# Optimization experiments

Measured on AMD Instinct MI355X. Metric: run time of the kernel, lower is better.

## Reference

```python
import jax, jax.numpy as jnp
import numpy as np

N_TOKENS = 16384
HIDDEN = 1024
FFN = 256
N_EXPERTS = 12
TOP_K = 3


def setup_inputs() -> dict:
    key = jax.random.key(0)
    ks = jax.random.split(key, 5)
    return {
        "hidden_states": jax.random.normal(ks[0], (N_TOKENS, HIDDEN), dtype=jnp.float32),
        "gate_w": jax.random.normal(ks[1], (N_EXPERTS, HIDDEN), dtype=jnp.float32) * 0.02,
        "w1": jax.random.normal(ks[2], (N_EXPERTS, FFN, HIDDEN), dtype=jnp.float32) * 0.02,
        "w2": jax.random.normal(ks[3], (N_EXPERTS, HIDDEN, FFN), dtype=jnp.float32) * 0.02,
        "w3": jax.random.normal(ks[4], (N_EXPERTS, FFN, HIDDEN), dtype=jnp.float32) * 0.02,
    }


def reference(hidden_states, gate_w, w1, w2, w3):
    # Eval mode: no jitter noise (module only applies it when self.training).
    n = hidden_states.shape[0]
    router_logits = hidden_states @ gate_w.T                       # [N, E]
    routing_weights = jax.nn.softmax(router_logits.astype(jnp.float32), axis=1)
    top_w, selected_experts = jax.lax.top_k(routing_weights, TOP_K)  # [N, K]
    top_w = top_w / jnp.sum(top_w, axis=-1, keepdims=True)
    top_w = top_w.astype(hidden_states.dtype)

    # Dense combine-weight matrix [N, E]: zero for unselected experts.
    combine = jnp.zeros((n, N_EXPERTS), dtype=hidden_states.dtype)
    combine = combine.at[jnp.arange(n)[:, None], selected_experts].add(top_w)

    # SwiGLU experts computed for all (token, expert) pairs; unselected pairs
    # are zeroed by the combine weights -> same math as gather/scatter loop.
    h1 = jnp.einsum('nd,efd->nef', hidden_states, w1)              # [N, E, F]
    h3 = jnp.einsum('nd,efd->nef', hidden_states, w3)              # [N, E, F]
    h = jax.nn.silu(h1) * h3
    h = h * combine[:, :, None]                                    # weight before combine
    final = jnp.einsum('nef,edf->nd', h, w2)                       # [N, D]

    flat_e = selected_experts.reshape(-1)
    flat_w = top_w.reshape(-1).astype(jnp.float32)
    importance = jnp.zeros((N_EXPERTS,), jnp.float32).at[flat_e].add(flat_w)
    # torch.std is unbiased (ddof=1)
    router_loss = jnp.std(importance, ddof=1)
    return final, router_logits, selected_experts, router_loss
```

## Files before the change

kernel.cpp:

```cpp
#include <hip/hip_runtime.h>
#include <hip/hip_bf16.h>

#define NT 16384
#define HID 1024
#define FFN_ 256
#define NE 12
#define TOPK 3

typedef float  float4x  __attribute__((ext_vector_type(4)));
typedef short  short8x  __attribute__((ext_vector_type(8)));

__device__ __forceinline__ unsigned short f2bf(float f) {
    unsigned u = __float_as_uint(f);
    u += 0x7fffu + ((u >> 16) & 1u);
    return (unsigned short)(u >> 16);
}
__device__ __forceinline__ float bf2f(unsigned short u) {
    return __uint_as_float(((unsigned)u) << 16);
}

__device__ __forceinline__ void gl2lds16(const void* g, void* l) {
    __builtin_amdgcn_global_load_lds(
        (const __attribute__((address_space(1))) unsigned int*)g,
        (__attribute__((address_space(3))) unsigned int*)l, 16, 0, 0);
}

__global__ __launch_bounds__(256) void router_cvt_kernel(
    const float* __restrict__ X, const float* __restrict__ G,
    const float* __restrict__ w1, const float* __restrict__ w3, const float* __restrict__ w2,
    unsigned short* __restrict__ o1, unsigned short* __restrict__ o3, unsigned short* __restrict__ o2,
    float* __restrict__ out_logits, float* __restrict__ out_sel,
    unsigned short* __restrict__ xb,
    int* __restrict__ sel_e, float* __restrict__ sel_w)
{
    __shared__ __align__(16) float gls[NE * HID];

    if (blockIdx.x < 768) {
        const float* s; unsigned short* d;
        int m = blockIdx.x >> 8;
        if (m == 0)      { s = w1; d = o1; }
        else if (m == 1) { s = w3; d = o3; }
        else             { s = w2; d = o2; }
        const int n4 = NE * FFN_ * HID / 4;
        for (int i = (blockIdx.x & 255) * 256 + threadIdx.x; i < n4; i += 65536) {
            float4 v = ((const float4*)s)[i];
            ushort4 o;
            o.x = f2bf(v.x); o.y = f2bf(v.y); o.z = f2bf(v.z); o.w = f2bf(v.w);
            ((ushort4*)d)[i] = o;
        }
        return;
    }

    const int bx = blockIdx.x - 768;
    for (int i = threadIdx.x; i < NE * HID / 4; i += 256)
        ((float4*)gls)[i] = ((const float4*)G)[i];
    __syncthreads();

    const int wave = threadIdx.x >> 6, lane = threadIdx.x & 63;
    const int t = bx * 4 + wave;

    float xr[16];
    const float* xt = X + (size_t)t * HID;
    unsigned short* xbt = xb + (size_t)t * HID;
#pragma unroll
    for (int j = 0; j < 4; j++) {
        float4 v = ((const float4*)xt)[j * 64 + lane];
        xr[j*4+0] = v.x; xr[j*4+1] = v.y; xr[j*4+2] = v.z; xr[j*4+3] = v.w;
        ushort4 o;
        o.x = f2bf(v.x); o.y = f2bf(v.y); o.z = f2bf(v.z); o.w = f2bf(v.w);
        ((ushort4*)xbt)[j * 64 + lane] = o;
    }

    float logit[NE];
#pragma unroll
    for (int e = 0; e < NE; e++) {
        float s = 0.f;
#pragma unroll
        for (int j = 0; j < 4; j++) {
            float4 g = ((const float4*)gls)[e * 256 + j * 64 + lane];
            s += xr[j*4+0]*g.x + xr[j*4+1]*g.y + xr[j*4+2]*g.z + xr[j*4+3]*g.w;
        }
#pragma unroll
        for (int d = 32; d; d >>= 1) s += __shfl_xor(s, d, 64);
        logit[e] = s;
    }

    if (lane == 0) {
        float m = logit[0];
#pragma unroll
        for (int e = 1; e < NE; e++) m = fmaxf(m, logit[e]);
#pragma unroll
        for (int e = 0; e < NE; e++) out_logits[(size_t)t * NE + e] = logit[e];

        bool used[NE];
#pragma unroll
        for (int e = 0; e < NE; e++) used[e] = false;
        int   sel[TOPK];
        float w[TOPK];
        float wsum = 0.f;
#pragma unroll
        for (int k = 0; k < TOPK; k++) {
            int best = -1; float bv = -1e30f;
            for (int e = 0; e < NE; e++)
                if (!used[e] && logit[e] > bv) { bv = logit[e]; best = e; }
            used[best] = true;
            sel[k] = best;
            w[k] = __expf(bv - m);
            wsum += w[k];
        }
        float inv = 1.f / wsum;
#pragma unroll
        for (int k = 0; k < TOPK; k++) {
            float wk = w[k] * inv;
            out_sel[(size_t)t * TOPK + k] = (float)sel[k];
            sel_e[t * TOPK + k] = sel[k];
            sel_w[t * TOPK + k] = wk;
        }
    }
}

__global__ __launch_bounds__(256) void hist_kernel(
    const int* __restrict__ sel_e, const float* __restrict__ sel_w,
    int* __restrict__ counts, float* __restrict__ importance)
{
    __shared__ int   lcnt[NE];
    __shared__ float limp[NE];
    const int tid = threadIdx.x;
    if (tid < NE) { lcnt[tid] = 0; limp[tid] = 0.f; }
    __syncthreads();
    const int t = blockIdx.x * 256 + tid;
#pragma unroll
    for (int k = 0; k < TOPK; k++) {
        int e = sel_e[t * TOPK + k];
        atomicAdd(&lcnt[e], 1);
        atomicAdd(&limp[e], sel_w[t * TOPK + k]);
    }
    __syncthreads();
    if (tid < NE) {
        atomicAdd(&counts[tid], lcnt[tid]);
        atomicAdd(&importance[tid], limp[tid]);
    }
}

__global__ void scan_loss(const int* __restrict__ counts, int* __restrict__ cursor,
                          int* __restrict__ offsets, const float* __restrict__ importance,
                          float* __restrict__ loss_out)
{
    if (threadIdx.x == 0) {
        int acc = 0;
        for (int e = 0; e < NE; e++) { offsets[e] = acc; cursor[e] = acc; acc += counts[e]; }
        offsets[NE] = acc;
        float mean = 0.f;
        for (int e = 0; e < NE; e++) mean += importance[e];
        mean /= (float)NE;
        float var = 0.f;
        for (int e = 0; e < NE; e++) { float d = importance[e] - mean; var += d * d; }
        var /= (float)(NE - 1);
        *loss_out = sqrtf(var);
    }
}

__global__ __launch_bounds__(256) void place_kernel(
    const int* __restrict__ sel_e, const float* __restrict__ sel_w,
    int* __restrict__ cursor, int* __restrict__ tok_ids, float* __restrict__ slot_w,
    int* __restrict__ inv3)
{
    __shared__ int lcnt[NE];
    __shared__ int lbase[NE];
    const int tid = threadIdx.x;
    if (tid < NE) lcnt[tid] = 0;
    __syncthreads();
    const int t = blockIdx.x * 256 + tid;
    int e[TOPK], r[TOPK];
#pragma unroll
    for (int k = 0; k < TOPK; k++) {
        e[k] = sel_e[t * TOPK + k];
        r[k] = atomicAdd(&lcnt[e[k]], 1);
    }
    __syncthreads();
    if (tid < NE) lbase[tid] = atomicAdd(&cursor[tid], lcnt[tid]);
    __syncthreads();
#pragma unroll
    for (int k = 0; k < TOPK; k++) {
        int pos = lbase[e[k]] + r[k];
        tok_ids[pos] = t;
        slot_w[pos] = sel_w[t * TOPK + k];
        inv3[t * TOPK + k] = pos;
    }
}

__global__ __launch_bounds__(256) void ffn1_kernel(
    const unsigned short* __restrict__ xb, const unsigned short* __restrict__ wb1,
    const unsigned short* __restrict__ wb3, const int* __restrict__ offsets,
    const int* __restrict__ tok_ids, const float* __restrict__ slot_w,
    unsigned short* __restrict__ H)
{
    const int e = blockIdx.z;
    const int base = offsets[e];
    const int count = offsets[e + 1] - base;
    const int m0 = blockIdx.x * 128;
    if (m0 >= count) return;
    const int n0 = blockIdx.y * 128;

    __shared__ __align__(16) unsigned short As[128 * 32];
    __shared__ __align__(16) unsigned short B1s[128 * 32];
    __shared__ __align__(16) unsigned short B3s[128 * 32];
    __shared__ int   tids[128];
    __shared__ float wts[128];

    const int tid = threadIdx.x;
    if (tid < 128) {
        int s = m0 + tid;
        tids[tid] = (s < count) ? tok_ids[base + s] : 0;
        wts[tid]  = (s < count) ? slot_w[base + s] : 0.f;
    }
    __syncthreads();

    const int wave = tid >> 6, lane = tid & 63;
    const int wave_m = wave & 1, wave_n = wave >> 1;

    const int srow = wave * 32 + (lane >> 2);
    const int schunk = (((lane & 3) ^ ((srow >> 1) & 3)) << 3);
    const int tokA0 = tids[srow];
    const int tokA1 = tids[srow + 16];

    const unsigned short* asrc0 = xb + (size_t)tokA0 * HID + schunk;
    const unsigned short* asrc1 = xb + (size_t)tokA1 * HID + schunk;
    const unsigned short* b1p0 = wb1 + (size_t)(e * FFN_ + n0 + srow) * HID + schunk;
    const unsigned short* b1p1 = b1p0 + 16 * HID;
    const unsigned short* b3p0 = wb3 + (size_t)(e * FFN_ + n0 + srow) * HID + schunk;
    const unsigned short* b3p1 = b3p0 + 16 * HID;

    char* aD0  = (char*)As  + wave * 2048;  char* aD1  = aD0 + 1024;
    char* b1D0 = (char*)B1s + wave * 2048;  char* b1D1 = b1D0 + 1024;
    char* b3D0 = (char*)B3s + wave * 2048;  char* b3D1 = b3D0 + 1024;

    const int r15 = lane & 15;
    const int rchunk = (((lane >> 4) ^ ((r15 >> 1) & 3)) << 3);

    float4x acc1[4][4], acc3[4][4];
#pragma unroll
    for (int mi = 0; mi < 4; mi++)
#pragma unroll
        for (int ni = 0; ni < 4; ni++) {
            acc1[mi][ni] = (float4x){0.f, 0.f, 0.f, 0.f};
            acc3[mi][ni] = (float4x){0.f, 0.f, 0.f, 0.f};
        }

    for (int kk = 0; kk < HID / 32; kk++) {
        __syncthreads();
        gl2lds16(asrc0, aD0);  gl2lds16(asrc1, aD1);
        gl2lds16(b1p0, b1D0);  gl2lds16(b1p1, b1D1);
        gl2lds16(b3p0, b3D0);  gl2lds16(b3p1, b3D1);
        __syncthreads();
        asrc0 += 32; asrc1 += 32; b1p0 += 32; b1p1 += 32; b3p0 += 32; b3p1 += 32;

        short8x a[4], b1f[4], b3f[4];
#pragma unroll
        for (int mi = 0; mi < 4; mi++)
            a[mi] = *(const short8x*)(As + (wave_m * 64 + mi * 16 + r15) * 32 + rchunk);
#pragma unroll
        for (int ni = 0; ni < 4; ni++) {
            b1f[ni] = *(const short8x*)(B1s + (wave_n * 64 + ni * 16 + r15) * 32 + rchunk);
            b3f[ni] = *(const short8x*)(B3s + (wave_n * 64 + ni * 16 + r15) * 32 + rchunk);
        }
#pragma unroll
        for (int mi = 0; mi < 4; mi++)
#pragma unroll
            for (int ni = 0; ni < 4; ni++) {
                acc1[mi][ni] = __builtin_amdgcn_mfma_f32_16x16x32_bf16(a[mi], b1f[ni], acc1[mi][ni], 0, 0, 0);
                acc3[mi][ni] = __builtin_amdgcn_mfma_f32_16x16x32_bf16(a[mi], b3f[ni], acc3[mi][ni], 0, 0, 0);
            }
    }

    const int laneh = lane >> 4;
#pragma unroll
    for (int mi = 0; mi < 4; mi++)
#pragma unroll
        for (int ni = 0; ni < 4; ni++)
#pragma unroll
            for (int r = 0; r < 4; r++) {
                int ml = wave_m * 64 + mi * 16 + laneh * 4 + r;
                int s = m0 + ml;
                if (s < count) {
                    float v1 = acc1[mi][ni][r];
                    float v3 = acc3[mi][ni][r];
                    float h = v1 * (1.f / (1.f + __expf(-v1))) * v3 * wts[ml];
                    int n = n0 + wave_n * 64 + ni * 16 + r15;
                    H[(size_t)(base + s) * FFN_ + n] = f2bf(h);
                }
            }
}

__global__ __launch_bounds__(256) void ffn2_store(
    const unsigned short* __restrict__ H, const unsigned short* __restrict__ wb2,
    const int* __restrict__ offsets, unsigned short* __restrict__ Obuf,
    int co, int nc)
{
    const int e = blockIdx.z;
    const int base = offsets[e];
    const int count = offsets[e + 1] - base;
    const int m0 = blockIdx.x * 128;
    if (m0 >= count) return;
    const int n0g = co + blockIdx.y * 128;

    __shared__ __align__(16) unsigned short As[128 * 32];
    __shared__ __align__(16) unsigned short Bs[128 * 32];

    const int tid = threadIdx.x;
    const int wave = tid >> 6, lane = tid & 63;
    const int wave_m = wave & 1, wave_n = wave >> 1;

    const int srow = wave * 32 + (lane >> 2);
    const int schunk = (((lane & 3) ^ ((srow >> 1) & 3)) << 3);

    const unsigned short* a0 = H + (size_t)(base + m0 + srow) * FFN_ + schunk;
    const unsigned short* a1 = a0 + 16 * FFN_;
    const unsigned short* b0 = wb2 + (size_t)(e * HID + n0g + srow) * FFN_ + schunk;
    const unsigned short* b1 = b0 + 16 * FFN_;

    char* aD0 = (char*)As + wave * 2048;  char* aD1 = aD0 + 1024;
    char* bD0 = (char*)Bs + wave * 2048;  char* bD1 = bD0 + 1024;

    const int r15 = lane & 15;
    const int rchunk = (((lane >> 4) ^ ((r15 >> 1) & 3)) << 3);

    float4x acc[4][4];
#pragma unroll
    for (int mi = 0; mi < 4; mi++)
#pragma unroll
        for (int ni = 0; ni < 4; ni++) acc[mi][ni] = (float4x){0.f, 0.f, 0.f, 0.f};

    for (int kk = 0; kk < FFN_ / 32; kk++) {
        __syncthreads();
        gl2lds16(a0, aD0);  gl2lds16(a1, aD1);
        gl2lds16(b0, bD0);  gl2lds16(b1, bD1);
        __syncthreads();
        a0 += 32; a1 += 32; b0 += 32; b1 += 32;

        short8x af[4], bf[4];
#pragma unroll
        for (int mi = 0; mi < 4; mi++)
            af[mi] = *(const short8x*)(As + (wave_m * 64 + mi * 16 + r15) * 32 + rchunk);
#pragma unroll
        for (int ni = 0; ni < 4; ni++)
            bf[ni] = *(const short8x*)(Bs + (wave_n * 64 + ni * 16 + r15) * 32 + rchunk);
#pragma unroll
        for (int mi = 0; mi < 4; mi++)
#pragma unroll
            for (int ni = 0; ni < 4; ni++)
                acc[mi][ni] = __builtin_amdgcn_mfma_f32_16x16x32_bf16(af[mi], bf[ni], acc[mi][ni], 0, 0, 0);
    }

    const int laneh = lane >> 4;
#pragma unroll
    for (int mi = 0; mi < 4; mi++)
#pragma unroll
        for (int ni = 0; ni < 4; ni++)
#pragma unroll
            for (int r = 0; r < 4; r++) {
                int ml = wave_m * 64 + mi * 16 + laneh * 4 + r;
                int s = m0 + ml;
                if (s < count) {
                    int col = (n0g - co) + wave_n * 64 + ni * 16 + r15;
                    Obuf[(size_t)(base + s) * nc + col] = f2bf(acc[mi][ni][r]);
                }
            }
}

__global__ __launch_bounds__(256) void combine_kernel(
    const unsigned short* __restrict__ Obuf, const int* __restrict__ inv3,
    float* __restrict__ final_out, int co, int pt_shift)
{
    const int idx = blockIdx.x * 256 + threadIdx.x;
    const int per_t = 1 << pt_shift;
    const int t = idx >> pt_shift;
    const int c4 = idx & (per_t - 1);
    const int s0 = inv3[t * TOPK + 0];
    const int s1 = inv3[t * TOPK + 1];
    const int s2 = inv3[t * TOPK + 2];
    const ushort4* O = (const ushort4*)Obuf;
    ushort4 u0 = O[(size_t)s0 * per_t + c4];
    ushort4 u1 = O[(size_t)s1 * per_t + c4];
    ushort4 u2 = O[(size_t)s2 * per_t + c4];
    float4 r;
    r.x = bf2f(u0.x) + bf2f(u1.x) + bf2f(u2.x);
    r.y = bf2f(u0.y) + bf2f(u1.y) + bf2f(u2.y);
    r.z = bf2f(u0.z) + bf2f(u1.z) + bf2f(u2.z);
    r.w = bf2f(u0.w) + bf2f(u1.w) + bf2f(u2.w);
    ((float4*)(final_out + (size_t)t * HID + co))[c4] = r;
}

__global__ __launch_bounds__(256) void ffn2_atomic(
    const unsigned short* __restrict__ H, const unsigned short* __restrict__ wb2,
    const int* __restrict__ offsets, const int* __restrict__ tok_ids,
    float* __restrict__ final_out)
{
    const int e = blockIdx.z;
    const int base = offsets[e];
    const int count = offsets[e + 1] - base;
    const int m0 = blockIdx.x * 128;
    if (m0 >= count) return;
    const int n0 = blockIdx.y * 128;

    __shared__ __align__(16) unsigned short As[128 * 32];
    __shared__ __align__(16) unsigned short Bs[128 * 32];
    __shared__ int tids[128];

    const int tid = threadIdx.x;
    if (tid < 128) {
        int s = m0 + tid;
        tids[tid] = (s < count) ? tok_ids[base + s] : 0;
    }
    __syncthreads();

    const int wave = tid >> 6, lane = tid & 63;
    const int wave_m = wave & 1, wave_n = wave >> 1;

    const int srow = wave * 32 + (lane >> 2);
    const int schunk = (((lane & 3) ^ ((srow >> 1) & 3)) << 3);
    const unsigned short* a0 = H + (size_t)(base + m0 + srow) * FFN_ + schunk;
    const unsigned short* a1 = a0 + 16 * FFN_;
    const unsigned short* b0 = wb2 + (size_t)(e * HID + n0 + srow) * FFN_ + schunk;
    const unsigned short* b1 = b0 + 16 * FFN_;

    char* aD0 = (char*)As + wave * 2048;  char* aD1 = aD0 + 1024;
    char* bD0 = (char*)Bs + wave * 2048;  char* bD1 = bD0 + 1024;

    const int r15 = lane & 15;
    const int rchunk = (((lane >> 4) ^ ((r15 >> 1) & 3)) << 3);

    float4x acc[4][4];
#pragma unroll
    for (int mi = 0; mi < 4; mi++)
#pragma unroll
        for (int ni = 0; ni < 4; ni++) acc[mi][ni] = (float4x){0.f, 0.f, 0.f, 0.f};

    for (int kk = 0; kk < FFN_ / 32; kk++) {
        __syncthreads();
        gl2lds16(a0, aD0);  gl2lds16(a1, aD1);
        gl2lds16(b0, bD0);  gl2lds16(b1, bD1);
        __syncthreads();
        a0 += 32; a1 += 32; b0 += 32; b1 += 32;

        short8x af[4], bf[4];
#pragma unroll
        for (int mi = 0; mi < 4; mi++)
            af[mi] = *(const short8x*)(As + (wave_m * 64 + mi * 16 + r15) * 32 + rchunk);
#pragma unroll
        for (int ni = 0; ni < 4; ni++)
            bf[ni] = *(const short8x*)(Bs + (wave_n * 64 + ni * 16 + r15) * 32 + rchunk);
#pragma unroll
        for (int mi = 0; mi < 4; mi++)
#pragma unroll
            for (int ni = 0; ni < 4; ni++)
                acc[mi][ni] = __builtin_amdgcn_mfma_f32_16x16x32_bf16(af[mi], bf[ni], acc[mi][ni], 0, 0, 0);
    }

    const int laneh = lane >> 4;
#pragma unroll
    for (int mi = 0; mi < 4; mi++)
#pragma unroll
        for (int ni = 0; ni < 4; ni++)
#pragma unroll
            for (int r = 0; r < 4; r++) {
                int ml = wave_m * 64 + mi * 16 + laneh * 4 + r;
                int s = m0 + ml;
                if (s < count) {
                    int n = n0 + wave_n * 64 + ni * 16 + r15;
                    atomicAdd(final_out + (size_t)tids[ml] * HID + n, acc[mi][ni][r]);
                }
            }
}

extern "C" void kernel_launch(void* const* d_in, const int* in_sizes, int n_in,
                              void* d_out, int out_size, void* d_ws, size_t ws_size,
                              hipStream_t stream) {
    const float* X  = (const float*)d_in[0];
    const float* G  = (const float*)d_in[1];
    const float* w1 = (const float*)d_in[2];
    const float* w2 = (const float*)d_in[3];
    const float* w3 = (const float*)d_in[4];

    float* out = (float*)d_out;
    float* out_final  = out;
    float* out_logits = out + (size_t)NT * HID;
    float* out_sel    = out_logits + (size_t)NT * NE;
    float* out_loss   = out_sel + (size_t)NT * TOPK;

    char* ws = (char*)d_ws;
    int*   counts     = (int*)(ws + 0);
    int*   cursor     = (int*)(ws + 64);
    int*   offsets    = (int*)(ws + 128);
    float* importance = (float*)(ws + 192);
    int*   sel_e   = (int*)(ws + 512);
    float* sel_w   = (float*)(ws + 197120);
    int*   tok_ids = (int*)(ws + 393728);
    float* slot_w  = (float*)(ws + 590336);
    unsigned short* wb1 = (unsigned short*)(ws + 786944);
    unsigned short* wb3 = (unsigned short*)(ws + 7078400);
    unsigned short* wb2 = (unsigned short*)(ws + 13369856);
    unsigned short* H   = (unsigned short*)(ws + 19661312);
    int*  inv3          = (int*)(ws + 44892672);
    const size_t obase  = 45089280;
    unsigned short* Obuf = (unsigned short*)(ws + obase);

    unsigned short* xb = (unsigned short*)d_out;

    int nc = 0;
    if      (ws_size >= obase + (size_t)NT * TOPK * 1024 * 2) nc = 1024;
    else if (ws_size >= obase + (size_t)NT * TOPK * 512  * 2) nc = 512;
    else if (ws_size >= obase + (size_t)NT * TOPK * 256  * 2) nc = 256;

    hipMemsetAsync(ws, 0, 256, stream);
    router_cvt_kernel<<<768 + NT / 4, 256, 0, stream>>>(
        X, G, w1, w3, w2, wb1, wb3, wb2, out_logits, out_sel, xb, sel_e, sel_w);
    hist_kernel<<<NT / 256, 256, 0, stream>>>(sel_e, sel_w, counts, importance);
    scan_loss<<<1, 64, 0, stream>>>(counts, cursor, offsets, importance, out_loss);
    place_kernel<<<NT / 256, 256, 0, stream>>>(sel_e, sel_w, cursor, tok_ids, slot_w, inv3);
    ffn1_kernel<<<dim3(48, 2, NE), 256, 0, stream>>>(xb, wb1, wb3, offsets, tok_ids, slot_w, H);

    if (nc) {
        const int np = 1024 / nc;
        const int pt_shift = (nc == 1024) ? 8 : (nc == 512 ? 7 : 6);
        for (int p = 0; p < np; p++) {
            ffn2_store<<<dim3(48, nc / 128, NE), 256, 0, stream>>>(
                H, wb2, offsets, Obuf, p * nc, nc);
            combine_kernel<<<(NT << pt_shift) / 256, 256, 0, stream>>>(
                Obuf, inv3, out_final, p * nc, pt_shift);
        }
    } else {
        hipMemsetAsync(d_out, 0, (size_t)NT * HID * sizeof(float), stream);
        ffn2_atomic<<<dim3(48, 8, NE), 256, 0, stream>>>(H, wb2, offsets, tok_ids, out_final);
    }
}
```

Baseline: 390.5 us.

## Double-buffer LDS tiles in expert GEMMs and compact grid via per-expert tile prefix

Each of the three expert GEMM kernels now uses two LDS stages. The next K-slice is loaded while the current one is consumed, removing one barrier per iteration. The launch grid is flattened to a compact list of 128-row tiles, using a tile_base prefix computed in scan_loss, so the many empty per-expert blocks are no longer launched. This doubles LDS per block and adds a small expert lookup loop per block.

```diff
diff --git a/kernel.cpp b/kernel.cpp
--- a/kernel.cpp
+++ b/kernel.cpp
@@ -143,13 +143,19 @@
 }
 
 __global__ void scan_loss(const int* __restrict__ counts, int* __restrict__ cursor,
-                          int* __restrict__ offsets, const float* __restrict__ importance,
+                          int* __restrict__ offsets, int* __restrict__ tile_base,
+                          const float* __restrict__ importance,
                           float* __restrict__ loss_out)
 {
     if (threadIdx.x == 0) {
-        int acc = 0;
-        for (int e = 0; e < NE; e++) { offsets[e] = acc; cursor[e] = acc; acc += counts[e]; }
+        int acc = 0, tb = 0;
+        for (int e = 0; e < NE; e++) {
+            offsets[e] = acc; cursor[e] = acc; tile_base[e] = tb;
+            tb += (counts[e] + 127) >> 7;
+            acc += counts[e];
+        }
         offsets[NE] = acc;
+        tile_base[NE] = tb;
         float mean = 0.f;
         for (int e = 0; e < NE; e++) mean += importance[e];
         mean /= (float)NE;
@@ -192,19 +198,22 @@
 __global__ __launch_bounds__(256) void ffn1_kernel(
     const unsigned short* __restrict__ xb, const unsigned short* __restrict__ wb1,
     const unsigned short* __restrict__ wb3, const int* __restrict__ offsets,
+    const int* __restrict__ tile_base,
     const int* __restrict__ tok_ids, const float* __restrict__ slot_w,
     unsigned short* __restrict__ H)
 {
-    const int e = blockIdx.z;
+    const int bx = blockIdx.x;
+    if (bx >= tile_base[NE]) return;
+    int e = 0;
+    while (bx >= tile_base[e + 1]) e++;
     const int base = offsets[e];
     const int count = offsets[e + 1] - base;
-    const int m0 = blockIdx.x * 128;
-    if (m0 >= count) return;
+    const int m0 = (bx - tile_base[e]) << 7;
     const int n0 = blockIdx.y * 128;
 
-    __shared__ __align__(16) unsigned short As[128 * 32];
-    __shared__ __align__(16) unsigned short B1s[128 * 32];
-    __shared__ __align__(16) unsigned short B3s[128 * 32];
+    __shared__ __align__(16) unsigned short As[2][4096];
+    __shared__ __align__(16) unsigned short B1s[2][4096];
+    __shared__ __align__(16) unsigned short B3s[2][4096];
     __shared__ int   tids[128];
     __shared__ float wts[128];
 
@@ -231,9 +240,17 @@
     const unsigned short* b3p0 = wb3 + (size_t)(e * FFN_ + n0 + srow) * HID + schunk;
     const unsigned short* b3p1 = b3p0 + 16 * HID;
 
-    char* aD0  = (char*)As  + wave * 2048;  char* aD1  = aD0 + 1024;
-    char* b1D0 = (char*)B1s + wave * 2048;  char* b1D1 = b1D0 + 1024;
-    char* b3D0 = (char*)B3s + wave * 2048;  char* b3D1 = b3D0 + 1024;
+    const int woff = wave * 2048;
+
+#define FFN1_STAGE(p) do {                                             \
+        char* aD  = (char*)&As[p][0]  + woff;                          \
+        char* b1D = (char*)&B1s[p][0] + woff;                          \
+        char* b3D = (char*)&B3s[p][0] + woff;                          \
+        gl2lds16(asrc0, aD);  gl2lds16(asrc1, aD + 1024);              \
+        gl2lds16(b1p0, b1D);  gl2lds16(b1p1, b1D + 1024);              \
+        gl2lds16(b3p0, b3D);  gl2lds16(b3p1, b3D + 1024);              \
+        asrc0 += 32; asrc1 += 32; b1p0 += 32; b1p1 += 32;              \
+        b3p0 += 32; b3p1 += 32; } while (0)
 
     const int r15 = lane & 15;
     const int rchunk = (((lane >> 4) ^ ((r15 >> 1) & 3)) << 3);
@@ -247,22 +264,20 @@
             acc3[mi][ni] = (float4x){0.f, 0.f, 0.f, 0.f};
         }
 
+    FFN1_STAGE(0);
     for (int kk = 0; kk < HID / 32; kk++) {
         __syncthreads();
-        gl2lds16(asrc0, aD0);  gl2lds16(asrc1, aD1);
-        gl2lds16(b1p0, b1D0);  gl2lds16(b1p1, b1D1);
-        gl2lds16(b3p0, b3D0);  gl2lds16(b3p1, b3D1);
-        __syncthreads();
-        asrc0 += 32; asrc1 += 32; b1p0 += 32; b1p1 += 32; b3p0 += 32; b3p1 += 32;
+        if (kk + 1 < HID / 32) FFN1_STAGE((kk + 1) & 1);
+        const int p = kk & 1;
 
         short8x a[4], b1f[4], b3f[4];
 #pragma unroll
         for (int mi = 0; mi < 4; mi++)
-            a[mi] = *(const short8x*)(As + (wave_m * 64 + mi * 16 + r15) * 32 + rchunk);
+            a[mi] = *(const short8x*)(&As[p][0] + (wave_m * 64 + mi * 16 + r15) * 32 + rchunk);
 #pragma unroll
         for (int ni = 0; ni < 4; ni++) {
-            b1f[ni] = *(const short8x*)(B1s + (wave_n * 64 + ni * 16 + r15) * 32 + rchunk);
-            b3f[ni] = *(const short8x*)(B3s + (wave_n * 64 + ni * 16 + r15) * 32 + rchunk);
+            b1f[ni] = *(const short8x*)(&B1s[p][0] + (wave_n * 64 + ni * 16 + r15) * 32 + rchunk);
+            b3f[ni] = *(const short8x*)(&B3s[p][0] + (wave_n * 64 + ni * 16 + r15) * 32 + rchunk);
         }
 #pragma unroll
         for (int mi = 0; mi < 4; mi++)
@@ -272,6 +287,7 @@
                 acc3[mi][ni] = __builtin_amdgcn_mfma_f32_16x16x32_bf16(a[mi], b3f[ni], acc3[mi][ni], 0, 0, 0);
             }
     }
+#undef FFN1_STAGE
 
     const int laneh = lane >> 4;
 #pragma unroll
@@ -294,18 +310,20 @@
 
 __global__ __launch_bounds__(256) void ffn2_store(
     const unsigned short* __restrict__ H, const unsigned short* __restrict__ wb2,
-    const int* __restrict__ offsets, unsigned short* __restrict__ Obuf,
-    int co, int nc)
-{
-    const int e = blockIdx.z;
+    const int* __restrict__ offsets, const int* __restrict__ tile_base,
+    unsigned short* __restrict__ Obuf, int co, int nc)
+{
+    const int bx = blockIdx.x;
+    if (bx >= tile_base[NE]) return;
+    int e = 0;
+    while (bx >= tile_base[e + 1]) e++;
     const int base = offsets[e];
     const int count = offsets[e + 1] - base;
-    const int m0 = blockIdx.x * 128;
-    if (m0 >= count) return;
+    const int m0 = (bx - tile_base[e]) << 7;
     const int n0g = co + blockIdx.y * 128;
 
-    __shared__ __align__(16) unsigned short As[128 * 32];
-    __shared__ __align__(16) unsigned short Bs[128 * 32];
+    __shared__ __align__(16) unsigned short As[2][4096];
+    __shared__ __align__(16) unsigned short Bs[2][4096];
 
     const int tid = threadIdx.x;
     const int wave = tid >> 6, lane = tid & 63;
@@ -319,8 +337,14 @@
     const unsigned short* b0 = wb2 + (size_t)(e * HID + n0g + srow) * FFN_ + schunk;
     const unsigned short* b1 = b0 + 16 * FFN_;
 
-    char* aD0 = (char*)As + wave * 2048;  char* aD1 = aD0 + 1024;
-    char* bD0 = (char*)Bs + wave * 2048;  char* bD1 = bD0 + 1024;
+    const int woff = wave * 2048;
+
+#define FFN2_STAGE(p) do {                                             \
+        char* aD = (char*)&As[p][0] + woff;                            \
+        char* bD = (char*)&Bs[p][0] + woff;                            \
+        gl2lds16(a0, aD);  gl2lds16(a1, aD + 1024);                    \
+        gl2lds16(b0, bD);  gl2lds16(b1, bD + 1024);                    \
+        a0 += 32; a1 += 32; b0 += 32; b1 += 32; } while (0)
 
     const int r15 = lane & 15;
     const int rchunk = (((lane >> 4) ^ ((r15 >> 1) & 3)) << 3);
@@ -331,26 +355,26 @@
 #pragma unroll
         for (int ni = 0; ni < 4; ni++) acc[mi][ni] = (float4x){0.f, 0.f, 0.f, 0.f};
 
+    FFN2_STAGE(0);
     for (int kk = 0; kk < FFN_ / 32; kk++) {
         __syncthreads();
-        gl2lds16(a0, aD0);  gl2lds16(a1, aD1);
-        gl2lds16(b0, bD0);  gl2lds16(b1, bD1);
-        __syncthreads();
-        a0 += 32; a1 += 32; b0 += 32; b1 += 32;
+        if (kk + 1 < FFN_ / 32) FFN2_STAGE((kk + 1) & 1);
+        const int p = kk & 1;
 
         short8x af[4], bf[4];
 #pragma unroll
         for (int mi = 0; mi < 4; mi++)
-            af[mi] = *(const short8x*)(As + (wave_m * 64 + mi * 16 + r15) * 32 + rchunk);
+            af[mi] = *(const short8x*)(&As[p][0] + (wave_m * 64 + mi * 16 + r15) * 32 + rchunk);
 #pragma unroll
         for (int ni = 0; ni < 4; ni++)
-            bf[ni] = *(const short8x*)(Bs + (wave_n * 64 + ni * 16 + r15) * 32 + rchunk);
+            bf[ni] = *(const short8x*)(&Bs[p][0] + (wave_n * 64 + ni * 16 + r15) * 32 + rchunk);
 #pragma unroll
         for (int mi = 0; mi < 4; mi++)
 #pragma unroll
             for (int ni = 0; ni < 4; ni++)
                 acc[mi][ni] = __builtin_amdgcn_mfma_f32_16x16x32_bf16(af[mi], bf[ni], acc[mi][ni], 0, 0, 0);
     }
+#undef FFN2_STAGE
 
     const int laneh = lane >> 4;
 #pragma unroll
@@ -393,18 +417,20 @@
 
 __global__ __launch_bounds__(256) void ffn2_atomic(
     const unsigned short* __restrict__ H, const unsigned short* __restrict__ wb2,
-    const int* __restrict__ offsets, const int* __restrict__ tok_ids,
-    float* __restrict__ final_out)
-{
-    const int e = blockIdx.z;
+    const int* __restrict__ offsets, const int* __restrict__ tile_base,
+    const int* __restrict__ tok_ids, float* __restrict__ final_out)
+{
+    const int bx = blockIdx.x;
+    if (bx >= tile_base[NE]) return;
+    int e = 0;
+    while (bx >= tile_base[e + 1]) e++;
     const int base = offsets[e];
     const int count = offsets[e + 1] - base;
-    const int m0 = blockIdx.x * 128;
-    if (m0 >= count) return;
+    const int m0 = (bx - tile_base[e]) << 7;
     const int n0 = blockIdx.y * 128;
 
-    __shared__ __align__(16) unsigned short As[128 * 32];
-    __shared__ __align__(16) unsigned short Bs[128 * 32];
+    __shared__ __align__(16) unsigned short As[2][4096];
+    __shared__ __align__(16) unsigned short Bs[2][4096];
     __shared__ int tids[128];
 
     const int tid = threadIdx.x;
@@ -424,8 +450,13 @@
     const unsigned short* b0 = wb2 + (size_t)(e * HID + n0 + srow) * FFN_ + schunk;
     const unsigned short* b1 = b0 + 16 * FFN_;
 
-    char* aD0 = (char*)As + wave * 2048;  char* aD1 = aD0 + 1024;
-    char* bD0 = (char*)Bs + wave * 2048;  char* bD1 = bD0 + 1024;
+    const int woff = wave * 2048;
+#define FFN2A_STAGE(p) do {                                            \
+        char* aD = (char*)&As[p][0] + woff;                            \
+        char* bD = (char*)&Bs[p][0] + woff;                            \
+        gl2lds16(a0, aD);  gl2lds16(a1, aD + 1024);                    \
+        gl2lds16(b0, bD);  gl2lds16(b1, bD + 1024);                    \
+        a0 += 32; a1 += 32; b0 += 32; b1 += 32; } while (0)
 
     const int r15 = lane & 15;
     const int rchunk = (((lane >> 4) ^ ((r15 >> 1) & 3)) << 3);
@@ -436,26 +467,25 @@
 #pragma unroll
         for (int ni = 0; ni < 4; ni++) acc[mi][ni] = (float4x){0.f, 0.f, 0.f, 0.f};
 
+    FFN2A_STAGE(0);
     for (int kk = 0; kk < FFN_ / 32; kk++) {
         __syncthreads();
-        gl2lds16(a0, aD0);  gl2lds16(a1, aD1);
-        gl2lds16(b0, bD0);  gl2lds16(b1, bD1);
-        __syncthreads();
-        a0 += 32; a1 += 32; b0 += 32; b1 += 32;
-
+        if (kk + 1 < FFN_ / 32) FFN2A_STAGE((kk + 1) & 1);
+        const int p = kk & 1;
         short8x af[4], bf[4];
 #pragma unroll
         for (int mi = 0; mi < 4; mi++)
-            af[mi] = *(const short8x*)(As + (wave_m * 64 + mi * 16 + r15) * 32 + rchunk);
+            af[mi] = *(const short8x*)(&As[p][0] + (wave_m * 64 + mi * 16 + r15) * 32 + rchunk);
 #pragma unroll
         for (int ni = 0; ni < 4; ni++)
-            bf[ni] = *(const short8x*)(Bs + (wave_n * 64 + ni * 16 + r15) * 32 + rchunk);
+            bf[ni] = *(const short8x*)(&Bs[p][0] + (wave_n * 64 + ni * 16 + r15) * 32 + rchunk);
 #pragma unroll
         for (int mi = 0; mi < 4; mi++)
 #pragma unroll
             for (int ni = 0; ni < 4; ni++)
                 acc[mi][ni] = __builtin_amdgcn_mfma_f32_16x16x32_bf16(af[mi], bf[ni], acc[mi][ni], 0, 0, 0);
     }
+#undef FFN2A_STAGE
 
     const int laneh = lane >> 4;
 #pragma unroll
@@ -493,6 +523,7 @@
     int*   cursor     = (int*)(ws + 64);
     int*   offsets    = (int*)(ws + 128);
     float* importance = (float*)(ws + 192);
+    int*   tile_base  = (int*)(ws + 256);
     int*   sel_e   = (int*)(ws + 512);
     float* sel_w   = (float*)(ws + 197120);
     int*   tok_ids = (int*)(ws + 393728);
@@ -512,25 +543,27 @@
     else if (ws_size >= obase + (size_t)NT * TOPK * 512  * 2) nc = 512;
     else if (ws_size >= obase + (size_t)NT * TOPK * 256  * 2) nc = 256;
 
-    hipMemsetAsync(ws, 0, 256, stream);
+    hipMemsetAsync(ws, 0, 320, stream);
     router_cvt_kernel<<<768 + NT / 4, 256, 0, stream>>>(
         X, G, w1, w3, w2, wb1, wb3, wb2, out_logits, out_sel, xb, sel_e, sel_w);
     hist_kernel<<<NT / 256, 256, 0, stream>>>(sel_e, sel_w, counts, importance);
-    scan_loss<<<1, 64, 0, stream>>>(counts, cursor, offsets, importance, out_loss);
+    scan_loss<<<1, 64, 0, stream>>>(counts, cursor, offsets, tile_base, importance, out_loss);
     place_kernel<<<NT / 256, 256, 0, stream>>>(sel_e, sel_w, cursor, tok_ids, slot_w, inv3);
-    ffn1_kernel<<<dim3(48, 2, NE), 256, 0, stream>>>(xb, wb1, wb3, offsets, tok_ids, slot_w, H);
+    ffn1_kernel<<<dim3(400, 2), 256, 0, stream>>>(xb, wb1, wb3, offsets, tile_base,
+                                                  tok_ids, slot_w, H);
 
     if (nc) {
         const int np = 1024 / nc;
         const int pt_shift = (nc == 1024) ? 8 : (nc == 512 ? 7 : 6);
         for (int p = 0; p < np; p++) {
-            ffn2_store<<<dim3(48, nc / 128, NE), 256, 0, stream>>>(
-                H, wb2, offsets, Obuf, p * nc, nc);
+            ffn2_store<<<dim3(400, nc / 128), 256, 0, stream>>>(
+                H, wb2, offsets, tile_base, Obuf, p * nc, nc);
             combine_kernel<<<(NT << pt_shift) / 256, 256, 0, stream>>>(
                 Obuf, inv3, out_final, p * nc, pt_shift);
         }
     } else {
         hipMemsetAsync(d_out, 0, (size_t)NT * HID * sizeof(float), stream);
-        ffn2_atomic<<<dim3(48, 8, NE), 256, 0, stream>>>(H, wb2, offsets, tok_ids, out_final);
-    }
-}
+        ffn2_atomic<<<dim3(400, 8), 256, 0, stream>>>(H, wb2, offsets, tile_base,
+                                                      tok_ids, out_final);
+    }
+}
```

Result: faster. 374.3 us (-4.2%).
